# Kernel optimization log

Measured on AMD Instinct MI355X. Metric: run time of the kernel, lower is better.

Reference implementation:

```python
import jax, jax.numpy as jnp
import numpy as np

B, TP, TH = 128, 128, 64
V, E, H, O = 50000, 300, 512, 3


def _lstm(x, lens, Wih, Whh, bih, bhh):
    # PyTorch LSTM, batch_first, gate order i,f,g,o; masked like pack_padded_sequence
    Bn, T, _ = x.shape
    Hn = Whh.shape[1]
    mask = jnp.arange(T)[None, :] < lens[:, None]  # [B,T]
    def step(carry, xt_mt):
        h, c = carry
        xt, mt = xt_mt  # [B,E], [B,1]
        g = xt @ Wih.T + h @ Whh.T + bih + bhh
        i, f, gg, o = jnp.split(g, 4, axis=-1)
        c_new = jax.nn.sigmoid(f) * c + jax.nn.sigmoid(i) * jnp.tanh(gg)
        h_new = jax.nn.sigmoid(o) * jnp.tanh(c_new)
        return (jnp.where(mt, h_new, h), jnp.where(mt, c_new, c)), jnp.where(mt, h_new, 0.0)
    z = jnp.zeros((Bn, Hn), x.dtype)
    _, hs = jax.lax.scan(step, (z, z), (jnp.swapaxes(x, 0, 1), jnp.swapaxes(mask, 0, 1)[..., None]))
    return jnp.swapaxes(hs, 0, 1)  # [B,T,H]


def _cell(x, h, c, Wih, Whh, bih, bhh):
    g = x @ Wih.T + h @ Whh.T + bih + bhh
    i, f, gg, o = jnp.split(g, 4, axis=-1)
    c_new = jax.nn.sigmoid(f) * c + jax.nn.sigmoid(i) * jnp.tanh(gg)
    h_new = jax.nn.sigmoid(o) * jnp.tanh(c_new)
    return h_new, c_new


def setup_inputs() -> dict:
    key = jax.random.key(0)
    ks = jax.random.split(key, 24)
    def unif(k, shape, fan):
        s = 1.0 / np.sqrt(fan)
        return jax.random.uniform(k, shape, jnp.float32, -s, s)
    inp = {}
    inp["premise"] = jax.random.randint(ks[0], (B, TP), 0, V, jnp.int32)
    inp["premise_len"] = jnp.full((B,), TP, jnp.int32)
    inp["hypothesis"] = jax.random.randint(ks[1], (B, TH), 0, V, jnp.int32)
    inp["hypothesis_len"] = jnp.full((B,), TH, jnp.int32)
    inp["embed_table"] = jax.random.normal(ks[2], (V, E), jnp.float32) * 0.1
    inp["embed_table"] = inp["embed_table"].at[0].set(0.0)  # padding_idx=0
    # premise LSTM
    inp["Wih_p"] = unif(ks[3], (4 * H, E), H); inp["Whh_p"] = unif(ks[4], (4 * H, H), H)
    inp["bih_p"] = unif(ks[5], (4 * H,), H); inp["bhh_p"] = unif(ks[6], (4 * H,), H)
    # hypothesis LSTM
    inp["Wih_h"] = unif(ks[7], (4 * H, E), H); inp["Whh_h"] = unif(ks[8], (4 * H, H), H)
    inp["bih_h"] = unif(ks[9], (4 * H,), H); inp["bhh_h"] = unif(ks[10], (4 * H,), H)
    # match LSTMCell (input 2H)
    inp["Wih_m"] = unif(ks[11], (4 * H, 2 * H), H); inp["Whh_m"] = unif(ks[12], (4 * H, H), H)
    inp["bih_m"] = unif(ks[13], (4 * H,), H); inp["bhh_m"] = unif(ks[14], (4 * H,), H)
    # attention
    inp["w_e"] = jax.random.uniform(ks[15], (H,), jnp.float32, 0.0, 1.0)
    inp["W_s"] = unif(ks[16], (H, H), H)
    inp["W_t"] = unif(ks[17], (H, H), H)
    inp["W_m"] = unif(ks[18], (H, H), H)
    inp["W_fc"] = unif(ks[19], (O, H), H)
    inp["b_fc"] = unif(ks[20], (O,), H)
    return inp


def reference(premise, premise_len, hypothesis, hypothesis_len, embed_table,
              Wih_p, Whh_p, bih_p, bhh_p, Wih_h, Whh_h, bih_h, bhh_h,
              Wih_m, Whh_m, bih_m, bhh_m, w_e, W_s, W_t, W_m, W_fc, b_fc):
    Bn = premise.shape[0]
    Hn = Whh_m.shape[1]
    p_emb = embed_table[premise]      # [B,Tp,E]
    h_emb = embed_table[hypothesis]   # [B,Th,E]
    h_s = _lstm(p_emb, premise_len, Wih_p, Whh_p, bih_p, bhh_p)      # [B,Tp,H]
    h_t = _lstm(h_emb, hypothesis_len, Wih_h, Whh_h, bih_h, bhh_h)   # [B,Th,H]
    Ws = jnp.einsum('bth,gh->btg', h_s, W_s)  # precompute w_s(h_s) once

    def step(carry, htk):
        h_m, c_m = carry
        q = htk @ W_t.T + h_m @ W_m.T                    # [B,H]
        s = jnp.tanh(Ws + q[:, None, :])                 # [B,Tp,H]
        e = s @ w_e                                      # [B,Tp]
        alpha = jax.nn.softmax(e, axis=1)                # softmax over premise positions
        a = jnp.einsum('bt,bth->bh', alpha, h_s)
        m_k = jnp.concatenate([a, htk], axis=1)          # [B,2H]
        h_m2, c_m2 = _cell(m_k, h_m, c_m, Wih_m, Whh_m, bih_m, bhh_m)
        return (h_m2, c_m2), h_m2

    z = jnp.zeros((Bn, Hn), h_s.dtype)
    _, hm_all = jax.lax.scan(step, (z, z), jnp.swapaxes(h_t, 0, 1))  # [Th,B,H]
    hm_all = jnp.swapaxes(hm_all, 0, 1)                              # [B,Th,H]
    idx = (hypothesis_len - 1).astype(jnp.int32)[:, None, None]
    last = jnp.take_along_axis(hm_all, idx, axis=1)[:, 0, :]         # last hidden per example
    return last @ W_fc.T + b_fc
```

## Files before the change

### kernel.cpp

```cpp
#include <hip/hip_runtime.h>

constexpr int BB = 128;
constexpr int TPp = 128;
constexpr int THh = 64;
constexpr int HH = 512;

constexpr size_t OFF_HS     = 0;
constexpr size_t SZ_HS      = (size_t)16384 * 512;
constexpr size_t OFF_HT     = OFF_HS + SZ_HS;
constexpr size_t SZ_HT      = (size_t)8192 * 512;
constexpr size_t OFF_WSM    = OFF_HT + SZ_HT;
constexpr size_t SZ_WSM     = (size_t)16384 * 512;
constexpr size_t OFF_WIHT_P = OFF_WSM + SZ_WSM;
constexpr size_t SZ_WIHT    = (size_t)304 * 2048;
constexpr size_t OFF_WIHT_H = OFF_WIHT_P + SZ_WIHT;
constexpr size_t OFF_WHHT_P = OFF_WIHT_H + SZ_WIHT;
constexpr size_t OFF_WHHT_H = OFF_WHHT_P + (size_t)512 * 2048;
constexpr size_t OFF_WB1T   = OFF_WHHT_H + (size_t)512 * 2048;
constexpr size_t OFF_WIA    = OFF_WB1T + (size_t)2560 * 1024;
constexpr size_t OFF_WEF    = OFF_WIA + (size_t)2048 * 512;
constexpr size_t OFF_BM     = OFF_WEF + 512;
constexpr size_t OFF_HC_P   = OFF_BM + 2048;
constexpr size_t OFF_HC_H   = OFF_HC_P + 2 * (size_t)BB * HH;
constexpr size_t OFF_C_P    = OFF_HC_H + 2 * (size_t)BB * HH;
constexpr size_t OFF_C_H    = OFF_C_P + (size_t)BB * HH;
constexpr size_t OFF_Q      = OFF_C_H + (size_t)BB * HH;
constexpr size_t OFF_GH     = OFF_Q + (size_t)BB * HH;
constexpr size_t OFF_A      = OFF_GH + (size_t)BB * 2048;
constexpr size_t OFF_HM     = OFF_A + (size_t)BB * HH;
constexpr size_t OFF_CM     = OFF_HM + (size_t)BB * HH;
constexpr size_t OFF_LAST   = OFF_CM + (size_t)BB * HH;
constexpr size_t OFF_BARP   = OFF_LAST + (size_t)BB * HH;
constexpr size_t OFF_BARH   = OFF_BARP + 2560;
constexpr size_t OFF_BARF   = OFF_BARH + 2560;
constexpr size_t OFF_BARM   = OFF_BARF + 4352;
constexpr size_t WS_FLOATS  = OFF_BARM + 4352;

__device__ __forceinline__ float sigmf(float x) { return 1.0f / (1.0f + __expf(-x)); }
__device__ __forceinline__ float tanh_f(float x) {
  float e = __expf(-2.0f * fabsf(x));
  float r = (1.0f - e) / (1.0f + e);
  return copysignf(r, x);
}

__device__ __forceinline__ float aload4(const float* p) {
  unsigned u = __hip_atomic_load((const unsigned*)p, __ATOMIC_RELAXED, __HIP_MEMORY_SCOPE_AGENT);
  return __uint_as_float(u);
}
__device__ __forceinline__ void astore4(float* p, float v) {
  __hip_atomic_store((unsigned*)p, __float_as_uint(v), __ATOMIC_RELAXED, __HIP_MEMORY_SCOPE_AGENT);
}
__device__ __forceinline__ float4 aload16(const float* p) {
  const unsigned long long* q = (const unsigned long long*)p;
  unsigned long long u0 = __hip_atomic_load(q, __ATOMIC_RELAXED, __HIP_MEMORY_SCOPE_AGENT);
  unsigned long long u1 = __hip_atomic_load(q + 1, __ATOMIC_RELAXED, __HIP_MEMORY_SCOPE_AGENT);
  union { unsigned long long u; float2 f; } c0, c1;
  c0.u = u0; c1.u = u1;
  float4 f; f.x = c0.f.x; f.y = c0.f.y; f.z = c1.f.x; f.w = c1.f.y;
  return f;
}
__device__ __forceinline__ void astore16(float* p, float4 v) {
  union { unsigned long long u; float2 f; } c0, c1;
  c0.f.x = v.x; c0.f.y = v.y; c1.f.x = v.z; c1.f.y = v.w;
  unsigned long long* q = (unsigned long long*)p;
  __hip_atomic_store(q, c0.u, __ATOMIC_RELAXED, __HIP_MEMORY_SCOPE_AGENT);
  __hip_atomic_store(q + 1, c1.u, __ATOMIC_RELAXED, __HIP_MEMORY_SCOPE_AGENT);
}

__device__ __forceinline__ void gbarD(unsigned* bar, int ep, int first, int n) {
  asm volatile("s_waitcnt vmcnt(0) lgkmcnt(0)" ::: "memory");
  __syncthreads();
  const int tid = threadIdx.x;
  const int rel = (int)blockIdx.x - first;
  if (tid == 0)
    __hip_atomic_store(bar + (size_t)rel * 16, (unsigned)ep,
                       __ATOMIC_RELAXED, __HIP_MEMORY_SCOPE_AGENT);
  if (rel == 0) {
    if (tid < n)
      while (__hip_atomic_load(bar + (size_t)tid * 16,
                               __ATOMIC_RELAXED, __HIP_MEMORY_SCOPE_AGENT) < (unsigned)ep)
        __builtin_amdgcn_s_sleep(1);
    __syncthreads();
    if (tid == 0)
      __hip_atomic_store(bar + (size_t)n * 16, (unsigned)ep,
                         __ATOMIC_RELAXED, __HIP_MEMORY_SCOPE_AGENT);
  } else if (tid == 0) {
    while (__hip_atomic_load(bar + (size_t)n * 16,
                             __ATOMIC_RELAXED, __HIP_MEMORY_SCOPE_AGENT) < (unsigned)ep)
      __builtin_amdgcn_s_sleep(1);
  }
  __syncthreads();
}

__device__ __forceinline__ float red4(float v) {
  v += __shfl_down(v, 16, 64);
  v += __shfl_down(v, 32, 64);
  return v;
}

__global__ void k_diag(float* out, float v) {
  int i = blockIdx.x * 64 + threadIdx.x;
  if (i < BB * 3) out[i] = v;
}

__global__ __launch_bounds__(256) void k_prep(float* ws,
    const float* Wih_p, const float* bih_p, const float* bhh_p,
    const float* Wih_h, const float* bih_h, const float* bhh_h,
    const float* Whh_p, const float* Whh_h,
    const float* Whh_m, const float* Wih_m, const float* bih_m, const float* bhh_m,
    const float* W_m, const float* W_t, const float* w_e) {
  size_t gid = (size_t)blockIdx.x * 256 + threadIdx.x;
  if (gid < SZ_WIHT) {
    int k = (int)(gid >> 11), r = (int)(gid & 2047);
    float v = (k < 300) ? Wih_p[(size_t)r * 300 + k]
            : (k == 303) ? (bih_p[r] + bhh_p[r]) : 0.f;
    ws[OFF_WIHT_P + gid] = v;
    return;
  }
  gid -= SZ_WIHT;
  if (gid < SZ_WIHT) {
    int k = (int)(gid >> 11), r = (int)(gid & 2047);
    float v = (k < 300) ? Wih_h[(size_t)r * 300 + k]
            : (k == 303) ? (bih_h[r] + bhh_h[r]) : 0.f;
    ws[OFF_WIHT_H + gid] = v;
    return;
  }
  gid -= SZ_WIHT;
  const size_t NT = (size_t)512 * 2048;
  if (gid < NT) {
    int c = (int)(gid >> 9), kk = (int)(gid & 511);
    int j = c >> 2, g = c & 3;
    ws[OFF_WHHT_P + gid] = Whh_p[(size_t)(g * 512 + j) * 512 + kk];
    return;
  }
  gid -= NT;
  if (gid < NT) {
    int c = (int)(gid >> 9), kk = (int)(gid & 511);
    int j = c >> 2, g = c & 3;
    ws[OFF_WHHT_H + gid] = Whh_h[(size_t)(g * 512 + j) * 512 + kk];
    return;
  }
  gid -= NT;
  if (gid < (size_t)2560 * 1024) {
    int c = (int)(gid >> 10), k = (int)(gid & 1023);
    float v;
    if (c < 512) {
      v = (k < 512) ? W_m[(size_t)c * 512 + k] : W_t[(size_t)c * 512 + (k - 512)];
    } else {
      int p = c - 512;
      int j = p >> 2, g = p & 3;
      int r = g * 512 + j;
      v = (k < 512) ? Whh_m[(size_t)r * 512 + k] : Wih_m[(size_t)r * 1024 + k];
    }
    ws[OFF_WB1T + gid] = v;
    return;
  }
  gid -= (size_t)2560 * 1024;
  if (gid < (size_t)2048 * 512) {
    int c = (int)(gid >> 9), k = (int)(gid & 511);
    int j = c >> 2, g = c & 3;
    ws[OFF_WIA + gid] = Wih_m[((size_t)g * 512 + j) * 1024 + k];
    return;
  }
  gid -= (size_t)2048 * 512;
  if (gid < 512) { ws[OFF_WEF + gid] = w_e[gid]; return; }
  gid -= 512;
  if (gid < 2048) { ws[OFF_BM + gid] = bih_m[gid] + bhh_m[gid]; return; }
  gid -= 2048;
  if (gid < (size_t)393216) { ws[OFF_HC_P + gid] = 0.f; return; }
  gid -= 393216;
  if (gid < (size_t)131072) { ws[OFF_HM + gid] = 0.f; return; }
  gid -= 131072;
  if (gid < 13824) { ws[OFF_BARP + gid] = 0.f; return; }
}

__global__ __launch_bounds__(256) void k_gemm(const float* __restrict__ A,
                                              const float* __restrict__ Bw, int ldb, int Kdim,
                                              int N, float* __restrict__ C, int ntilesN) {
  __shared__ float As[16][68];
  __shared__ float Bs[16][68];
  const int tid = threadIdx.x;
  const int bid = blockIdx.x;
  const int tm = bid / ntilesN, tn = bid % ntilesN;
  const int m0 = tm * 64, n0 = tn * 64;
  const int tx = tid & 15, ty = tid >> 4;
  const int srow = tid >> 2, skc = (tid & 3) * 4;
  float acc[4][4] = {};
  const float* arowf = A + (size_t)(m0 + srow) * Kdim;
  const float* brow = Bw + (size_t)(n0 + srow) * ldb;
  for (int k0 = 0; k0 < Kdim; k0 += 16) {
    float4 v = *(const float4*)(arowf + k0 + skc);
    As[skc + 0][srow] = v.x; As[skc + 1][srow] = v.y;
    As[skc + 2][srow] = v.z; As[skc + 3][srow] = v.w;
#pragma unroll
    for (int i = 0; i < 4; i++) Bs[skc + i][srow] = brow[k0 + skc + i];
    __syncthreads();
#pragma unroll
    for (int kk = 0; kk < 16; kk++) {
      float4 a4 = *(float4*)&As[kk][ty * 4];
      float4 b4 = *(float4*)&Bs[kk][tx * 4];
      acc[0][0] += a4.x * b4.x; acc[0][1] += a4.x * b4.y; acc[0][2] += a4.x * b4.z; acc[0][3] += a4.x * b4.w;
      acc[1][0] += a4.y * b4.x; acc[1][1] += a4.y * b4.y; acc[1][2] += a4.y * b4.z; acc[1][3] += a4.y * b4.w;
      acc[2][0] += a4.z * b4.x; acc[2][1] += a4.z * b4.y; acc[2][2] += a4.z * b4.z; acc[2][3] += a4.z * b4.w;
      acc[3][0] += a4.w * b4.x; acc[3][1] += a4.w * b4.y; acc[3][2] += a4.w * b4.z; acc[3][3] += a4.w * b4.w;
    }
    __syncthreads();
  }
  const int m = m0 + ty * 4, n = n0 + tx * 4;
#pragma unroll
  for (int i = 0; i < 4; i++) {
    float4 o = {acc[i][0], acc[i][1], acc[i][2], acc[i][3]};
    *(float4*)&C[(size_t)(m + i) * N + n] = o;
  }
}

__global__ __launch_bounds__(512) void k_lstm_mega(float* __restrict__ ws,
    const int* __restrict__ premise, const int* __restrict__ hyp,
    const int* __restrict__ plen, const int* __restrict__ hlen,
    const float* __restrict__ emb) {
  __shared__ float4 smem4[4096];
  float4* Alds4 = smem4;
  float* xAs = (float*)(smem4 + 2048);
  float* xBs = xAs + 16 * 68;
  int* xTok = (int*)(xBs + 16 * 68);

  const int tid = threadIdx.x;
  const int bid = blockIdx.x;
  const int seq = bid >> 7;
  const int u = bid & 127;
  const int gb = u >> 4, gj = u & 15;
  const int T = seq ? THh : TPp;
  const int* toks = seq ? hyp : premise;
  const int* lens = seq ? hlen : plen;
  const float* WL = ws + (seq ? OFF_WHHT_H : OFF_WHHT_P);
  const float* WX = ws + (seq ? OFF_WIHT_H : OFF_WIHT_P);
  float* hc = ws + (seq ? OFF_HC_H : OFF_HC_P);
  float* hsout = ws + (seq ? OFF_HT : OFF_HS);
  float* xgd = ws + OFF_WSM + (size_t)(seq * 8 + gb) * (16 * 16 * 2048);
  unsigned* bar = (unsigned*)(ws + (seq ? OFF_BARH : OFF_BARP)) + gb * 272;
  const int dfirst = seq * 128 + gb * 16;

  const int w = tid >> 6, lane = tid & 63;
  const int b_loc = lane & 15, kq = lane >> 4;
  const int b_glob = gb * 16 + b_loc;
  const int c0 = gj * 128 + w * 16;
  const int j0 = c0 >> 2;
  const int len = lens[b_glob];
  float c_r[4] = {0.f, 0.f, 0.f, 0.f}, h_r[4] = {0.f, 0.f, 0.f, 0.f};
  int ep = 1;

  for (int t = 0; t < T; t++) {
    if ((t & 15) == 0) {
      for (int ti = gj; ti < 128; ti += 16) {
        const int tm = ti >> 5, tn = ti & 31;
        const int m0 = tm * 64, n0 = tn * 64;
        if (tid < 64) {
          int rr = m0 + tid;
          int tl = rr >> 4, bl = rr & 15;
          xTok[tid] = toks[(size_t)(gb * 16 + bl) * T + t + tl];
        }
        __syncthreads();
        const int sr = tid & 63, sk2 = (tid >> 6) * 2;
        const int tx = tid & 15, ty = tid >> 4;
        float acc2[2][4] = {};
        for (int k0 = 0; k0 < 304; k0 += 16) {
          int tok = xTok[sr];
#pragma unroll
          for (int i = 0; i < 2; i++) {
            int kx = k0 + sk2 + i;
            float v = 0.f;
            if (kx < 300) v = emb[(size_t)tok * 300 + kx];
            else if (kx == 303) v = 1.0f;
            xAs[(sk2 + i) * 68 + sr] = v;
          }
#pragma unroll
          for (int s = 0; s < 2; s++) {
            int i2 = tid + s * 512;
            int kb = i2 >> 6, nb = i2 & 63;
            xBs[kb * 68 + nb] = WX[(size_t)(k0 + kb) * 2048 + n0 + nb];
          }
          __syncthreads();
#pragma unroll
          for (int kk = 0; kk < 16; kk++) {
            float a0 = xAs[kk * 68 + ty * 2];
            float a1 = xAs[kk * 68 + ty * 2 + 1];
            float4 b4 = *(float4*)&xBs[kk * 68 + tx * 4];
            acc2[0][0] += a0 * b4.x; acc2[0][1] += a0 * b4.y; acc2[0][2] += a0 * b4.z; acc2[0][3] += a0 * b4.w;
            acc2[1][0] += a1 * b4.x; acc2[1][1] += a1 * b4.y; acc2[1][2] += a1 * b4.z; acc2[1][3] += a1 * b4.w;
          }
          __syncthreads();
        }
#pragma unroll
        for (int i = 0; i < 2; i++) {
          int rr = m0 + ty * 2 + i;
          int tl = rr >> 4, bl = rr & 15;
          float* dst = xgd + ((size_t)tl * 16 + bl) * 2048;
#pragma unroll
          for (int jj = 0; jj < 4; jj++) {
            int cI = n0 + tx * 4 + jj;
            int g = cI >> 9, j = cI & 511;
            astore4(dst + j * 4 + g, acc2[i][jj]);
          }
        }
      }
      gbarD(bar, ep, dfirst, 16); ep++;
    }
    {
      const float* hin = hc + (size_t)(t & 1) * (BB * HH);
      float* hout = hc + (size_t)((t + 1) & 1) * (BB * HH);
#pragma unroll
      for (int i = 0; i < 4; i++) {
        int f = tid + 512 * i;
        int bl = f >> 7, k4 = f & 127;
        Alds4[bl * 128 + (k4 ^ (bl & 7))] = aload16(hin + (size_t)(gb * 16 + bl) * 512 + k4 * 4);
      }
      __syncthreads();
      float acc[16];
#pragma unroll
      for (int c = 0; c < 16; c++) acc[c] = 0.f;
      for (int it = 0; it < 32; it++) {
        int kk = it * 16 + kq * 4;
        float4 a4 = Alds4[b_loc * 128 + ((it * 4 + kq) ^ (b_loc & 7))];
#pragma unroll
        for (int cq = 0; cq < 16; cq++) {
          float4 w4 = *(const float4*)&WL[(size_t)(c0 + cq) * 512 + kk];
          acc[cq] += a4.x * w4.x + a4.y * w4.y + a4.z * w4.z + a4.w * w4.w;
        }
      }
#pragma unroll
      for (int cq = 0; cq < 16; cq++) acc[cq] = red4(acc[cq]);
      if (kq == 0) {
        const float* xb = xgd + ((size_t)(t & 15) * 16 + b_loc) * 2048 + c0;
        float4 hv;
        float* hvp = (float*)&hv;
        bool inr = t < len;
#pragma unroll
        for (int jl = 0; jl < 4; jl++) {
          float4 xa = aload16(xb + jl * 4);
          float iv = sigmf(acc[jl * 4 + 0] + xa.x);
          float fv = sigmf(acc[jl * 4 + 1] + xa.y);
          float gv = tanh_f(acc[jl * 4 + 2] + xa.z);
          float ov = sigmf(acc[jl * 4 + 3] + xa.w);
          float cn = fv * c_r[jl] + iv * gv;
          float hn = ov * tanh_f(cn);
          if (inr) { c_r[jl] = cn; h_r[jl] = hn; }
          hvp[jl] = inr ? hn : 0.f;
        }
        *(float4*)(hsout + ((size_t)b_glob * T + t) * 512 + j0) = hv;
        float4 ho = {h_r[0], h_r[1], h_r[2], h_r[3]};
        astore16(hout + (size_t)b_glob * 512 + j0, ho);
      }
      gbarD(bar, ep, dfirst, 16); ep++;
    }
  }
}

__global__ __launch_bounds__(512) void k_match_mega(float* __restrict__ ws,
                                                    const int* __restrict__ hlen) {
  __shared__ float4 smem4[4096];
  float4* A1 = smem4;
  float4* A3 = smem4;
  float* SC = (float*)smem4;

  const int tid = threadIdx.x;
  const int bid = blockIdx.x;
  const int gr = bid >> 5, gc = bid & 31;
  const int dfirst = gr * 32;
  unsigned* bar = (unsigned*)(ws + OFF_BARM) + gr * 528;

  float* hm = ws + OFF_HM;
  const float* ht = ws + OFF_HT;
  float* q = ws + OFF_Q;
  float* gh = ws + OFF_GH;
  float* abuf = ws + OFF_A;
  float* last = ws + OFF_LAST;
  const float* B1 = ws + OFF_WB1T;
  const float* W3 = ws + OFF_WIA;

  const int w = tid >> 6, lane = tid & 63;
  const int rl = lane & 15, kq = lane >> 4;
  const int r_g = gr * 16 + rl;
  const int c0p = gc * 80 + w * 10;
  const int c0q = gc * 64 + w * 8;
  const int jq = c0q >> 2;
  float c_reg[2] = {0.f, 0.f};
  const int hl = hlen[r_g];
  float bmp[8];
#pragma unroll
  for (int jl = 0; jl < 2; jl++)
#pragma unroll
    for (int g = 0; g < 4; g++) bmp[jl * 4 + g] = ws[OFF_BM + g * 512 + jq + jl];
  int ep = 1;

  for (int k = 0; k < THh; k++) {
    {
#pragma unroll
      for (int i = 0; i < 8; i++) {
        int f = tid + 512 * i;
        int rr = f >> 8, k4 = f & 255;
        float4 v;
        if (k4 < 128) v = aload16(&hm[(size_t)(gr * 16 + rr) * 512 + k4 * 4]);
        else v = *(const float4*)&ht[((size_t)(gr * 16 + rr) * THh + k) * 512 + (k4 - 128) * 4];
        A1[rr * 256 + (k4 ^ (rr & 7))] = v;
      }
      __syncthreads();
      float acc[10];
#pragma unroll
      for (int cc = 0; cc < 10; cc++) acc[cc] = 0.f;
      for (int it = 0; it < 64; it++) {
        int kk = it * 16 + kq * 4;
        float4 a4 = A1[rl * 256 + ((it * 4 + kq) ^ (rl & 7))];
#pragma unroll
        for (int cc = 0; cc < 10; cc++) {
          float4 b4 = *(const float4*)&B1[(size_t)(c0p + cc) * 1024 + kk];
          acc[cc] += a4.x * b4.x + a4.y * b4.y + a4.z * b4.z + a4.w * b4.w;
        }
      }
#pragma unroll
      for (int cc = 0; cc < 10; cc++) acc[cc] = red4(acc[cc]);
      if (kq == 0) {
#pragma unroll
        for (int cc = 0; cc < 10; cc++) {
          int c = c0p + cc;
          if (c < 512) astore4(&q[(size_t)r_g * 512 + c], acc[cc]);
          else astore4(&gh[(size_t)r_g * 2048 + (c - 512)], acc[cc]);
        }
      }
    }
    gbarD(bar, ep, dfirst, 32); ep++;
    if (gc < 16) {
      const int b = gr * 16 + gc;
      float* q_lds = SC; float* we_lds = SC + 512; float* e_part = SC + 1024;
      float* e_lds = SC + 1536; float* alpha_lds = SC + 1664; float* red_s = SC + 1792;
      const float* Wsb = ws + OFF_WSM;
      const float* hs = ws + OFF_HS;
      q_lds[tid] = aload4(&q[(size_t)b * 512 + tid]);
      we_lds[tid] = ws[OFF_WEF + tid];
      __syncthreads();
      {
        int t2 = tid >> 2;
        int gbase = (tid & 3) * 128;
        const float* wsrow = Wsb + ((size_t)b * TPp + t2) * 512 + gbase;
        float s = 0.f;
        for (int ii = 0; ii < 128; ii += 4) {
          float4 wv = *(const float4*)(wsrow + ii);
          float4 qv = *(float4*)&q_lds[gbase + ii];
          float4 ev = *(float4*)&we_lds[gbase + ii];
          s += tanh_f(wv.x + qv.x) * ev.x + tanh_f(wv.y + qv.y) * ev.y +
               tanh_f(wv.z + qv.z) * ev.z + tanh_f(wv.w + qv.w) * ev.w;
        }
        e_part[tid] = s;
      }
      __syncthreads();
      if (tid < 128)
        e_lds[tid] = e_part[tid * 4] + e_part[tid * 4 + 1] + e_part[tid * 4 + 2] + e_part[tid * 4 + 3];
      __syncthreads();
      if (tid < 64) {
        float m = fmaxf(e_lds[tid], e_lds[tid + 64]);
        for (int off = 32; off > 0; off >>= 1) m = fmaxf(m, __shfl_down(m, off));
        if (tid == 0) red_s[0] = m;
      }
      __syncthreads();
      if (tid < 128) alpha_lds[tid] = __expf(e_lds[tid] - red_s[0]);
      __syncthreads();
      if (tid < 64) {
        float s = alpha_lds[tid] + alpha_lds[tid + 64];
        for (int off = 32; off > 0; off >>= 1) s += __shfl_down(s, off);
        if (tid == 0) red_s[1] = 1.f / s;
      }
      __syncthreads();
      {
        float inv = red_s[1];
        float a0 = 0.f;
        const float* hsb = hs + (size_t)b * TPp * 512 + tid;
        for (int t2 = 0; t2 < TPp; t2++) a0 += alpha_lds[t2] * hsb[(size_t)t2 * 512];
        astore4(&abuf[(size_t)b * 512 + tid], a0 * inv);
      }
    }
    gbarD(bar, ep, dfirst, 32); ep++;
    {
#pragma unroll
      for (int i = 0; i < 4; i++) {
        int f = tid + 512 * i;
        int rr = f >> 7, k4 = f & 127;
        A3[rr * 128 + (k4 ^ (rr & 7))] = aload16(&abuf[(size_t)(gr * 16 + rr) * 512 + k4 * 4]);
      }
      __syncthreads();
      float acc[8];
#pragma unroll
      for (int cc = 0; cc < 8; cc++) acc[cc] = 0.f;
      for (int it = 0; it < 32; it++) {
        int kk = it * 16 + kq * 4;
        float4 a4 = A3[rl * 128 + ((it * 4 + kq) ^ (rl & 7))];
#pragma unroll
        for (int cc = 0; cc < 8; cc++) {
          float4 w4 = *(const float4*)&W3[(size_t)(c0q + cc) * 512 + kk];
          acc[cc] += a4.x * w4.x + a4.y * w4.y + a4.z * w4.z + a4.w * w4.w;
        }
      }
#pragma unroll
      for (int cc = 0; cc < 8; cc++) acc[cc] = red4(acc[cc]);
      if (kq == 0) {
#pragma unroll
        for (int jl = 0; jl < 2; jl++) {
          float4 gh4 = aload16(&gh[(size_t)r_g * 2048 + c0q + jl * 4]);
          float iv = sigmf(acc[jl * 4 + 0] + gh4.x + bmp[jl * 4 + 0]);
          float fv = sigmf(acc[jl * 4 + 1] + gh4.y + bmp[jl * 4 + 1]);
          float gv = tanh_f(acc[jl * 4 + 2] + gh4.z + bmp[jl * 4 + 2]);
          float ov = sigmf(acc[jl * 4 + 3] + gh4.w + bmp[jl * 4 + 3]);
          float cn = fv * c_reg[jl] + iv * gv;
          float hn = ov * tanh_f(cn);
          c_reg[jl] = cn;
          astore4(&hm[(size_t)r_g * 512 + jq + jl], hn);
          if (k == hl - 1) last[(size_t)r_g * 512 + jq + jl] = hn;
        }
      }
    }
    gbarD(bar, ep, dfirst, 32); ep++;
  }
}

__global__ __launch_bounds__(256) void k_fc(const float* __restrict__ ws, const float* __restrict__ Wfc,
                                            const float* __restrict__ bfc, float* __restrict__ out) {
  int idx = blockIdx.x * 256 + threadIdx.x;
  if (idx >= BB * 3) return;
  int b = idx / 3, o = idx - b * 3;
  const float* lrow = ws + OFF_LAST + (size_t)b * 512;
  const float* wrow = Wfc + (size_t)o * 512;
  float acc = bfc[o];
  for (int h = 0; h < 512; h++) acc += lrow[h] * wrow[h];
  out[idx] = acc;
}

extern "C" void kernel_launch(void* const* d_in, const int* in_sizes, int n_in, void* d_out,
                              int out_size, void* d_ws, size_t ws_size, hipStream_t stream) {
  const int* premise = (const int*)d_in[0];
  const int* plen = (const int*)d_in[1];
  const int* hyp = (const int*)d_in[2];
  const int* hlen = (const int*)d_in[3];
  const float* emb = (const float*)d_in[4];
  const float* Wih_p = (const float*)d_in[5];
  const float* Whh_p = (const float*)d_in[6];
  const float* bih_p = (const float*)d_in[7];
  const float* bhh_p = (const float*)d_in[8];
  const float* Wih_h = (const float*)d_in[9];
  const float* Whh_h = (const float*)d_in[10];
  const float* bih_h = (const float*)d_in[11];
  const float* bhh_h = (const float*)d_in[12];
  const float* Wih_m = (const float*)d_in[13];
  const float* Whh_m = (const float*)d_in[14];
  const float* bih_m = (const float*)d_in[15];
  const float* bhh_m = (const float*)d_in[16];
  const float* w_e = (const float*)d_in[17];
  const float* W_s = (const float*)d_in[18];
  const float* W_t = (const float*)d_in[19];
  const float* W_m = (const float*)d_in[20];
  const float* W_fc = (const float*)d_in[21];
  const float* b_fc = (const float*)d_in[22];
  float* ws = (float*)d_ws;
  float* out = (float*)d_out;

  if (ws_size < WS_FLOATS * sizeof(float)) {
    float mb = (float)((double)ws_size / (1024.0 * 1024.0));
    k_diag<<<dim3(6), dim3(64), 0, stream>>>(out, mb);
    return;
  }

  {
    size_t total = 2 * SZ_WIHT + 2 * (size_t)512 * 2048 + (size_t)2560 * 1024 +
                   (size_t)2048 * 512 + 512 + 2048 + 393216 + 131072 + 13824;
    int nb = (int)((total + 255) / 256);
    k_prep<<<dim3(nb), dim3(256), 0, stream>>>(ws, Wih_p, bih_p, bhh_p, Wih_h, bih_h, bhh_h,
                                               Whh_p, Whh_h, Whh_m, Wih_m, bih_m, bhh_m,
                                               W_m, W_t, w_e);
  }
  {
    void* args[] = {(void*)&ws, (void*)&premise, (void*)&hyp, (void*)&plen, (void*)&hlen, (void*)&emb};
    hipError_t e = hipLaunchCooperativeKernel((const void*)k_lstm_mega, dim3(256), dim3(512),
                                              args, 0, stream);
    if (e != hipSuccess)
      k_lstm_mega<<<dim3(256), dim3(512), 0, stream>>>(ws, premise, hyp, plen, hlen, emb);
  }
  k_gemm<<<dim3(256 * 8), dim3(256), 0, stream>>>(ws + OFF_HS, W_s, 512, 512, 512,
                                                  ws + OFF_WSM, 8);
  {
    void* args[] = {(void*)&ws, (void*)&hlen};
    hipError_t e = hipLaunchCooperativeKernel((const void*)k_match_mega, dim3(256), dim3(512),
                                              args, 0, stream);
    if (e != hipSuccess)
      k_match_mega<<<dim3(256), dim3(512), 0, stream>>>(ws, hlen);
  }
  k_fc<<<dim3(2), dim3(256), 0, stream>>>(ws, W_fc, b_fc, out);
}
```

Before: 13.06 ms.

## Make input-projection chunks block-local to drop a grid barrier per 16 steps

The input-projection weights are re-permuted in prep so each block's 128 gate columns are contiguous in gate-interleaved order. Each block then computes exactly the x-gate projections it consumes, writes them to a private buffer with plain float4 stores, and skips the group-wide barrier that previously followed each 16-step chunk. The LDS allocation is halved by aliasing the h tile with the GEMM staging buffers. The cost is that each block now does the full 128x128 projection tile for its own columns, which adds no redundant work, but it needs extra __syncthreads to protect the aliased shared memory.

```diff
diff --git a/kernel.cpp b/kernel.cpp
--- a/kernel.cpp
+++ b/kernel.cpp
@@ -111,17 +111,21 @@
     const float* W_m, const float* W_t, const float* w_e) {
   size_t gid = (size_t)blockIdx.x * 256 + threadIdx.x;
   if (gid < SZ_WIHT) {
-    int k = (int)(gid >> 11), r = (int)(gid & 2047);
-    float v = (k < 300) ? Wih_p[(size_t)r * 300 + k]
-            : (k == 303) ? (bih_p[r] + bhh_p[r]) : 0.f;
+    int k = (int)(gid >> 11), c = (int)(gid & 2047);
+    int j = c >> 2, g = c & 3;
+    int row = g * 512 + j;
+    float v = (k < 300) ? Wih_p[(size_t)row * 300 + k]
+            : (k == 303) ? (bih_p[row] + bhh_p[row]) : 0.f;
     ws[OFF_WIHT_P + gid] = v;
     return;
   }
   gid -= SZ_WIHT;
   if (gid < SZ_WIHT) {
-    int k = (int)(gid >> 11), r = (int)(gid & 2047);
-    float v = (k < 300) ? Wih_h[(size_t)r * 300 + k]
-            : (k == 303) ? (bih_h[r] + bhh_h[r]) : 0.f;
+    int k = (int)(gid >> 11), c = (int)(gid & 2047);
+    int j = c >> 2, g = c & 3;
+    int row = g * 512 + j;
+    float v = (k < 300) ? Wih_h[(size_t)row * 300 + k]
+            : (k == 303) ? (bih_h[row] + bhh_h[row]) : 0.f;
     ws[OFF_WIHT_H + gid] = v;
     return;
   }
@@ -218,9 +222,8 @@
     const int* __restrict__ premise, const int* __restrict__ hyp,
     const int* __restrict__ plen, const int* __restrict__ hlen,
     const float* __restrict__ emb) {
-  __shared__ float4 smem4[4096];
-  float4* Alds4 = smem4;
-  float* xAs = (float*)(smem4 + 2048);
+  __shared__ float4 smem4[2048];
+  float* xAs = (float*)smem4;
   float* xBs = xAs + 16 * 68;
   int* xTok = (int*)(xBs + 16 * 68);
 
@@ -233,10 +236,10 @@
   const int* toks = seq ? hyp : premise;
   const int* lens = seq ? hlen : plen;
   const float* WL = ws + (seq ? OFF_WHHT_H : OFF_WHHT_P);
-  const float* WX = ws + (seq ? OFF_WIHT_H : OFF_WIHT_P);
+  const float* WXp = ws + (seq ? OFF_WIHT_H : OFF_WIHT_P);
   float* hc = ws + (seq ? OFF_HC_H : OFF_HC_P);
   float* hsout = ws + (seq ? OFF_HT : OFF_HS);
-  float* xgd = ws + OFF_WSM + (size_t)(seq * 8 + gb) * (16 * 16 * 2048);
+  float* xgb = ws + OFF_WSM + (size_t)bid * 32768;
   unsigned* bar = (unsigned*)(ws + (seq ? OFF_BARH : OFF_BARP)) + gb * 272;
   const int dfirst = seq * 128 + gb * 16;
 
@@ -251,17 +254,18 @@
 
   for (int t = 0; t < T; t++) {
     if ((t & 15) == 0) {
-      for (int ti = gj; ti < 128; ti += 16) {
-        const int tm = ti >> 5, tn = ti & 31;
-        const int m0 = tm * 64, n0 = tn * 64;
+      __syncthreads();
+      const int sr = tid & 63, sk2 = (tid >> 6) * 2;
+      const int tx = tid & 15, ty = tid >> 4;
+      for (int ti = 0; ti < 8; ti++) {
+        const int m0 = (ti >> 1) * 64;
+        const int cb = (ti & 1) * 64;
         if (tid < 64) {
           int rr = m0 + tid;
           int tl = rr >> 4, bl = rr & 15;
           xTok[tid] = toks[(size_t)(gb * 16 + bl) * T + t + tl];
         }
         __syncthreads();
-        const int sr = tid & 63, sk2 = (tid >> 6) * 2;
-        const int tx = tid & 15, ty = tid >> 4;
         float acc2[2][4] = {};
         for (int k0 = 0; k0 < 304; k0 += 16) {
           int tok = xTok[sr];
@@ -277,7 +281,7 @@
           for (int s = 0; s < 2; s++) {
             int i2 = tid + s * 512;
             int kb = i2 >> 6, nb = i2 & 63;
-            xBs[kb * 68 + nb] = WX[(size_t)(k0 + kb) * 2048 + n0 + nb];
+            xBs[kb * 68 + nb] = WXp[(size_t)(k0 + kb) * 2048 + gj * 128 + cb + nb];
           }
           __syncthreads();
 #pragma unroll
@@ -294,16 +298,11 @@
         for (int i = 0; i < 2; i++) {
           int rr = m0 + ty * 2 + i;
           int tl = rr >> 4, bl = rr & 15;
-          float* dst = xgd + ((size_t)tl * 16 + bl) * 2048;
-#pragma unroll
-          for (int jj = 0; jj < 4; jj++) {
-            int cI = n0 + tx * 4 + jj;
-            int g = cI >> 9, j = cI & 511;
-            astore4(dst + j * 4 + g, acc2[i][jj]);
-          }
-        }
-      }
-      gbarD(bar, ep, dfirst, 16); ep++;
+          float4 o = {acc2[i][0], acc2[i][1], acc2[i][2], acc2[i][3]};
+          *(float4*)&xgb[((size_t)tl * 16 + bl) * 128 + cb + tx * 4] = o;
+        }
+        __syncthreads();
+      }
     }
     {
       const float* hin = hc + (size_t)(t & 1) * (BB * HH);
@@ -312,7 +311,7 @@
       for (int i = 0; i < 4; i++) {
         int f = tid + 512 * i;
         int bl = f >> 7, k4 = f & 127;
-        Alds4[bl * 128 + (k4 ^ (bl & 7))] = aload16(hin + (size_t)(gb * 16 + bl) * 512 + k4 * 4);
+        smem4[bl * 128 + (k4 ^ (bl & 7))] = aload16(hin + (size_t)(gb * 16 + bl) * 512 + k4 * 4);
       }
       __syncthreads();
       float acc[16];
@@ -320,7 +319,7 @@
       for (int c = 0; c < 16; c++) acc[c] = 0.f;
       for (int it = 0; it < 32; it++) {
         int kk = it * 16 + kq * 4;
-        float4 a4 = Alds4[b_loc * 128 + ((it * 4 + kq) ^ (b_loc & 7))];
+        float4 a4 = smem4[b_loc * 128 + ((it * 4 + kq) ^ (b_loc & 7))];
 #pragma unroll
         for (int cq = 0; cq < 16; cq++) {
           float4 w4 = *(const float4*)&WL[(size_t)(c0 + cq) * 512 + kk];
@@ -330,13 +329,13 @@
 #pragma unroll
       for (int cq = 0; cq < 16; cq++) acc[cq] = red4(acc[cq]);
       if (kq == 0) {
-        const float* xb = xgd + ((size_t)(t & 15) * 16 + b_loc) * 2048 + c0;
+        const float* xb = xgb + ((size_t)(t & 15) * 16 + b_loc) * 128 + w * 16;
         float4 hv;
         float* hvp = (float*)&hv;
         bool inr = t < len;
 #pragma unroll
         for (int jl = 0; jl < 4; jl++) {
-          float4 xa = aload16(xb + jl * 4);
+          float4 xa = *(const float4*)(xb + jl * 4);
           float iv = sigmf(acc[jl * 4 + 0] + xa.x);
           float fv = sigmf(acc[jl * 4 + 1] + xa.y);
           float gv = tanh_f(acc[jl * 4 + 2] + xa.z);
```

Result: faster. 12.43 ms (-4.9%).
